# Kernel optimization log

Hardware: AMD Instinct MI355X
Metric: run time of the kernel (lower is better)

The kernel has to match this reference:

```python
import jax, jax.numpy as jnp
import numpy as np

B, N0, C, E, OUT = 64, 2048, 128, 2097152, 16


def setup_inputs() -> dict:
    key = jax.random.key(0)
    ks = jax.random.split(key, 16)
    s = 1.0 / np.sqrt(C)
    inp = {
        "x": jax.random.normal(ks[0], (B * N0, C), jnp.float32),
        "src_l": jax.random.randint(ks[1], (E,), 0, N0, jnp.int32),
        "dst_l": jax.random.randint(ks[2], (E,), 0, N0, jnp.int32),
        "g": jax.random.randint(ks[3], (E,), 0, B, jnp.int32),
    }
    for i in range(3):
        inp[f"W{i+1}"] = jax.random.normal(ks[4 + i], (C, C), jnp.float32) * s
        inp[f"b{i+1}"] = jnp.zeros((C,), jnp.float32)
        inp[f"p{i+1}"] = jax.random.normal(ks[7 + i], (C,), jnp.float32)
    inp["Wm"] = jax.random.normal(ks[10], (C, OUT), jnp.float32) * s
    inp["bm"] = jnp.zeros((OUT,), jnp.float32)
    return inp


def _gcn_conv(x, W, b, src, dst, ew, N):
    # PyG GCNConv: gcn_norm with self-loops (weight 1), symmetric D^-1/2 A D^-1/2
    xw = x @ W                                              # [N, C]
    deg = jnp.zeros((N,), xw.dtype).at[dst].add(ew) + 1.0   # +1 self-loop
    dis = jax.lax.rsqrt(deg)
    norm = dis[src] * ew * dis[dst]                         # [E]
    out = jnp.zeros_like(xw).at[dst].add(norm[:, None] * xw[src])
    out = out + xw / deg[:, None]                           # self-loop term: deg^-1
    return out + b


def _topk_pool(x, p, g, sl, dl, ew, k):
    # x: [B, n, C]; score = tanh(x.p/||p||); keep top-k nodes per graph
    n = x.shape[1]
    score = jnp.tanh(x @ (p / jnp.linalg.norm(p)))          # [B, n]
    vals, idx = jax.lax.top_k(score, k)                     # [B, k]
    xk = jnp.take_along_axis(x, idx[..., None], axis=1) * vals[..., None]
    mapping = jnp.full((x.shape[0], n), -1, jnp.int32).at[
        jnp.arange(x.shape[0])[:, None], idx
    ].set(jnp.arange(k, dtype=jnp.int32)[None, :])
    ns, nd = mapping[g, sl], mapping[g, dl]
    valid = (ew > 0) & (ns >= 0) & (nd >= 0)                # filter_adj as mask
    return xk, jnp.maximum(ns, 0), jnp.maximum(nd, 0), valid.astype(x.dtype)


def _forward(x, src_l, dst_l, g, params, Wm, bm):
    n = N0
    sl, dl = src_l, dst_l
    ew = jnp.ones(sl.shape, x.dtype)
    h = x
    for (W, b, p) in params:
        N = B * n
        src = g * n + sl
        dst = g * n + dl
        h = jax.nn.relu(_gcn_conv(h.reshape(N, -1), W, b, src, dst, ew, N))
        k = n // 2
        h, sl, dl, ew = _topk_pool(h.reshape(B, n, -1), p, g, sl, dl, ew, k)
        n = k
    pooled = h.sum(axis=1)                                  # global_add_pool -> [B, C]
    return pooled @ Wm + bm                                 # MLP([C, OUT], norm=None)


def reference(x, src_l, dst_l, g, W1, b1, p1, W2, b2, p2, W3, b3, p3, Wm, bm):
    return _forward(x, src_l, dst_l, g,
                    [(W1, b1, p1), (W2, b2, p2), (W3, b3, p3)], Wm, bm)
```

## Files before the change

### kernel.cpp

```cpp
#include <hip/hip_runtime.h>
#include <math.h>

#define BQ   64
#define NN0  2048
#define CF   128
#define ET   2097152
#define OUTF 16

static __device__ __forceinline__ unsigned f2o(float f) {
    unsigned u = __float_as_uint(f);
    return (u & 0x80000000u) ? ~u : (u | 0x80000000u);
}

__global__ void k_normp(const float* p1, const float* p2, const float* p3, float* pn) {
    const float* ps[3] = {p1, p2, p3};
    const float* p = ps[blockIdx.x];
    int t = threadIdx.x;
    float v = p[t];
    float s = v * v;
    for (int o = 32; o > 0; o >>= 1) s += __shfl_down(s, o);
    __shared__ float ws2[2];
    if ((t & 63) == 0) ws2[t >> 6] = s;
    __syncthreads();
    float tot = ws2[0] + ws2[1];
    pn[blockIdx.x * CF + t] = v / sqrtf(tot);
}

__global__ __launch_bounds__(256, 2) void k_gemm(const float* __restrict__ X,
                                                 const float* __restrict__ W,
                                                 float* __restrict__ Y, int N) {
    __shared__ float xT[32][260];
    __shared__ float Wc[32][128];
    int t = threadIdx.x;
    int cg = t & 15, rg = t >> 4;
    int c0 = cg * 8, r0 = rg * 16;
    int rowBase = blockIdx.x * 256;

    float acc[16][8];
#pragma unroll
    for (int i = 0; i < 16; i++)
#pragma unroll
        for (int j = 0; j < 8; j++) acc[i][j] = 0.f;

    for (int kc = 0; kc < 4; kc++) {
        __syncthreads();
#pragma unroll
        for (int j = 0; j < 8; j++) {
            int id = t + 256 * j;
            int r = id >> 3;
            int k4 = id & 7;
            float4 v = *(const float4*)&X[(rowBase + r) * CF + kc * 32 + k4 * 4];
            int kk = k4 * 4;
            xT[kk + 0][r] = v.x; xT[kk + 1][r] = v.y;
            xT[kk + 2][r] = v.z; xT[kk + 3][r] = v.w;
        }
#pragma unroll
        for (int j = 0; j < 4; j++) {
            int id = t + 256 * j;
            int kk = id >> 5;
            int cc = (id & 31) * 4;
            *(float4*)&Wc[kk][cc] = *(const float4*)&W[(kc * 32 + kk) * CF + cc];
        }
        __syncthreads();
#pragma unroll 4
        for (int kk = 0; kk < 32; kk++) {
            float xr[16];
#pragma unroll
            for (int i = 0; i < 16; i += 4)
                *(float4*)&xr[i] = *(float4*)&xT[kk][r0 + i];
            float wv[8];
            *(float4*)&wv[0] = *(float4*)&Wc[kk][c0];
            *(float4*)&wv[4] = *(float4*)&Wc[kk][c0 + 4];
#pragma unroll
            for (int i = 0; i < 16; i++)
#pragma unroll
                for (int j = 0; j < 8; j++)
                    acc[i][j] = fmaf(xr[i], wv[j], acc[i][j]);
        }
    }
#pragma unroll
    for (int i = 0; i < 16; i++) {
        int r = rowBase + r0 + i;
        *(float4*)&Y[r * CF + c0]     = make_float4(acc[i][0], acc[i][1], acc[i][2], acc[i][3]);
        *(float4*)&Y[r * CF + c0 + 4] = make_float4(acc[i][4], acc[i][5], acc[i][6], acc[i][7]);
    }
}

__global__ void k_hist1(const int* __restrict__ g, const int* __restrict__ dl, int* cnt) {
    int e = blockIdx.x * 256 + threadIdx.x;
    if (e < ET) atomicAdd(&cnt[g[e] * NN0 + dl[e]], 1);
}
__global__ void k_hist2(const int2* __restrict__ edges, const int* pE, int* cnt) {
    int e = blockIdx.x * 256 + threadIdx.x;
    if (e < *pE) atomicAdd(&cnt[edges[e].y], 1);
}

__global__ void k_ps1(const int* __restrict__ cnt, int* part) {
    int b = blockIdx.x, t = threadIdx.x;
    int base = b * 1024;
    int s = 0;
    for (int j = t; j < 1024; j += 256) s += cnt[base + j];
    for (int o = 32; o > 0; o >>= 1) s += __shfl_down(s, o);
    __shared__ int sm[4];
    if ((t & 63) == 0) sm[t >> 6] = s;
    __syncthreads();
    if (t == 0) part[b] = sm[0] + sm[1] + sm[2] + sm[3];
}
__global__ void k_ps3f(const int* __restrict__ cnt, const int* __restrict__ part,
                       int* rowS, int* curs, float* dis, int N, int nb) {
    __shared__ int pp[128];
    __shared__ int sm[256];
    int b = blockIdx.x, t = threadIdx.x;
    if (t < 128) pp[t] = (t < nb) ? part[t] : 0;
    __syncthreads();
    for (int o = 1; o < 128; o <<= 1) {
        int u = (t < 128 && t >= o) ? pp[t - o] : 0;
        __syncthreads();
        if (t < 128) pp[t] += u;
        __syncthreads();
    }
    int myBase = (b == 0) ? 0 : pp[b - 1];
    __syncthreads();

    int base = b * 1024;
    int loc[4], cv[4];
    int s = 0;
#pragma unroll
    for (int j = 0; j < 4; j++) { loc[j] = s; cv[j] = cnt[base + t * 4 + j]; s += cv[j]; }
    sm[t] = s;
    __syncthreads();
    for (int o = 1; o < 256; o <<= 1) {
        int u = (t >= o) ? sm[t - o] : 0;
        __syncthreads();
        sm[t] += u;
        __syncthreads();
    }
    int incl = sm[t];
    int thrBase = myBase + incl - s;
#pragma unroll
    for (int j = 0; j < 4; j++) {
        int idx = base + t * 4 + j;
        rowS[idx] = thrBase + loc[j];
        curs[idx] = thrBase + loc[j];
        if (dis != nullptr) dis[idx] = rsqrtf((float)(cv[j] + 1));
    }
    if (b == gridDim.x - 1 && t == 255) rowS[N] = myBase + incl;
}
__global__ void k_wscan(const int* __restrict__ wcnt, int* __restrict__ wbase) {
    __shared__ int sm[1024];
    int t = threadIdx.x;
    int base = t * 32;
    int v[32];
    int s = 0;
#pragma unroll
    for (int j = 0; j < 32; j++) { v[j] = s; s += wcnt[base + j]; }
    sm[t] = s;
    __syncthreads();
    for (int o = 1; o < 1024; o <<= 1) {
        int u = (t >= o) ? sm[t - o] : 0;
        __syncthreads();
        sm[t] += u;
        __syncthreads();
    }
    int ex = sm[t] - s;
#pragma unroll
    for (int j = 0; j < 32; j++) wbase[base + j] = ex + v[j];
    if (t == 1023) wbase[32768] = sm[1023];
}

__global__ void k_fill1(const int* __restrict__ g, const int* __restrict__ sl,
                        const int* __restrict__ dl, int* curs, int* csrS) {
    int r = blockIdx.x & 7;
    int base = (blockIdx.x >> 3) * 2048;
#pragma unroll
    for (int i = 0; i < 8; i++) {
        int e = base + i * 256 + threadIdx.x;
        int gg = g[e];
        int d = gg * NN0 + dl[e];
        if ((d >> 14) == r) {
            int pos = atomicAdd(&curs[d], 1);
            csrS[pos] = gg * NN0 + sl[e];
        }
    }
}
__global__ void k_fill2(const int2* __restrict__ edges, const int* pE,
                        int* curs, int* csrS, int shift) {
    int r = blockIdx.x & 7;
    int base = (blockIdx.x >> 3) * 2048;
    int E = *pE;
#pragma unroll
    for (int i = 0; i < 8; i++) {
        int e = base + i * 256 + threadIdx.x;
        if (e < E) {
            int2 ed = edges[e];
            if ((ed.y >> shift) == r) {
                int pos = atomicAdd(&curs[ed.y], 1);
                csrS[pos] = ed.x;
            }
        }
    }
}

__global__ void k_agg(const float4* __restrict__ xw, const int* __restrict__ rowS,
                      const int* __restrict__ csrS, const float* __restrict__ dis,
                      const float* __restrict__ bias, const float* __restrict__ pn,
                      float4* __restrict__ h, float* __restrict__ scores, int N) {
    int nb = gridDim.x;
    int bid = blockIdx.x;
    int sb = (bid & 7) * (nb >> 3) + (bid >> 3);
    int d = sb * 4 + (threadIdx.x >> 6);
    int lane = threadIdx.x & 63;
    int hl = lane >> 5;
    int l = lane & 31;
    int rs = rowS[d], re = rowS[d + 1];
    float4 a = make_float4(0.f, 0.f, 0.f, 0.f);
    for (int j0 = rs; j0 < re; j0 += 64) {
        int myj = j0 + lane;
        int sV = (myj < re) ? csrS[myj] : 0;
        float dV = (myj < re) ? dis[sV] : 0.f;
        int c64 = re - j0; if (c64 > 64) c64 = 64;
        int j = 0;
        for (; j + 8 <= c64; j += 8) {
            int i0 = j + hl, i1 = j + 2 + hl, i2 = j + 4 + hl, i3 = j + 6 + hl;
            int s0 = __shfl(sV, i0), s1 = __shfl(sV, i1);
            int s2 = __shfl(sV, i2), s3 = __shfl(sV, i3);
            float d0 = __shfl(dV, i0), d1 = __shfl(dV, i1);
            float d2 = __shfl(dV, i2), d3 = __shfl(dV, i3);
            float4 v0 = xw[s0 * 32 + l];
            float4 v1 = xw[s1 * 32 + l];
            float4 v2 = xw[s2 * 32 + l];
            float4 v3 = xw[s3 * 32 + l];
            a.x = fmaf(d0, v0.x, a.x); a.y = fmaf(d0, v0.y, a.y);
            a.z = fmaf(d0, v0.z, a.z); a.w = fmaf(d0, v0.w, a.w);
            a.x = fmaf(d1, v1.x, a.x); a.y = fmaf(d1, v1.y, a.y);
            a.z = fmaf(d1, v1.z, a.z); a.w = fmaf(d1, v1.w, a.w);
            a.x = fmaf(d2, v2.x, a.x); a.y = fmaf(d2, v2.y, a.y);
            a.z = fmaf(d2, v2.z, a.z); a.w = fmaf(d2, v2.w, a.w);
            a.x = fmaf(d3, v3.x, a.x); a.y = fmaf(d3, v3.y, a.y);
            a.z = fmaf(d3, v3.z, a.z); a.w = fmaf(d3, v3.w, a.w);
        }
        for (; j < c64; j += 2) {
            int i = j + hl;
            int ic = (i < c64) ? i : (c64 - 1);
            int s = __shfl(sV, ic);
            float dd = __shfl(dV, ic);
            if (i >= c64) dd = 0.f;
            float4 v = xw[s * 32 + l];
            a.x = fmaf(dd, v.x, a.x); a.y = fmaf(dd, v.y, a.y);
            a.z = fmaf(dd, v.z, a.z); a.w = fmaf(dd, v.w, a.w);
        }
    }
    a.x += __shfl_xor(a.x, 32);
    a.y += __shfl_xor(a.y, 32);
    a.z += __shfl_xor(a.z, 32);
    a.w += __shfl_xor(a.w, 32);
    float disd = dis[d];
    float invd = disd * disd;
    float4 xd = xw[d * 32 + l];
    float4 bv = ((const float4*)bias)[l];
    float4 r;
    r.x = disd * a.x + xd.x * invd + bv.x;
    r.y = disd * a.y + xd.y * invd + bv.y;
    r.z = disd * a.z + xd.z * invd + bv.z;
    r.w = disd * a.w + xd.w * invd + bv.w;
    r.x = r.x > 0.f ? r.x : 0.f;
    r.y = r.y > 0.f ? r.y : 0.f;
    r.z = r.z > 0.f ? r.z : 0.f;
    r.w = r.w > 0.f ? r.w : 0.f;
    if (hl == 0) h[d * 32 + l] = r;
    float4 pv = ((const float4*)pn)[l];
    float v = r.x * pv.x + r.y * pv.y + r.z * pv.z + r.w * pv.w;
    for (int o = 32; o > 0; o >>= 1) v += __shfl_down(v, o);
    if (lane == 0) scores[d] = tanhf(0.5f * v);
}

__global__ void k_topk(const float* __restrict__ scores, int* __restrict__ map, int n, int k) {
    __shared__ unsigned keys[2048];
    __shared__ int sm[256];
    __shared__ int red[4];
    int b = blockIdx.x, t = threadIdx.x;
    const float* sc = scores + b * n;
    int m = n >> 8;

    for (int i = t; i < n; i += 256) keys[i] = f2o(sc[i]);
    __syncthreads();

    unsigned prefix = 0u;
    for (int bit = 31; bit >= 0; bit--) {
        unsigned trial = prefix | (1u << bit);
        int c = 0;
        for (int i = t; i < n; i += 256) c += (keys[i] >= trial) ? 1 : 0;
        for (int o = 32; o > 0; o >>= 1) c += __shfl_down(c, o);
        if ((t & 63) == 0) red[t >> 6] = c;
        __syncthreads();
        int tot = red[0] + red[1] + red[2] + red[3];
        __syncthreads();
        if (tot >= k) prefix = trial;
    }
    unsigned T = prefix;

    int c = 0;
    for (int i = t; i < n; i += 256) c += (keys[i] > T) ? 1 : 0;
    for (int o = 32; o > 0; o >>= 1) c += __shfl_down(c, o);
    if ((t & 63) == 0) red[t >> 6] = c;
    __syncthreads();
    int mEq = k - (red[0] + red[1] + red[2] + red[3]);
    __syncthreads();

    int base = t * m;
    int eqc = 0;
    for (int j = 0; j < m; j++) eqc += (keys[base + j] == T) ? 1 : 0;
    sm[t] = eqc;
    __syncthreads();
    for (int o = 1; o < 256; o <<= 1) {
        int u = (t >= o) ? sm[t - o] : 0;
        __syncthreads();
        sm[t] += u;
        __syncthreads();
    }
    int er = sm[t] - eqc;
    __syncthreads();

    unsigned kb = 0; int kc = 0;
    for (int j = 0; j < m; j++) {
        unsigned ky = keys[base + j];
        bool kp = (ky > T) || (ky == T && er < mEq);
        if (ky == T) er++;
        if (kp) { kb |= (1u << j); kc++; }
    }
    sm[t] = kc;
    __syncthreads();
    for (int o = 1; o < 256; o <<= 1) {
        int u = (t >= o) ? sm[t - o] : 0;
        __syncthreads();
        sm[t] += u;
        __syncthreads();
    }
    int nidx = sm[t] - kc;
    for (int j = 0; j < m; j++) {
        map[b * n + base + j] = ((kb >> j) & 1u) ? nidx++ : -1;
    }
}

__global__ void k_compact(const float* __restrict__ h, const float* __restrict__ scores,
                          const int* __restrict__ map, float* __restrict__ xn,
                          int N, int n, int k) {
    int wid = (blockIdx.x * 256 + threadIdx.x) >> 6;
    int lane = threadIdx.x & 63;
    int mi = map[wid];
    if (mi < 0) return;
    float s = scores[wid];
    int gg = wid / n;
    int dst = (gg * k + mi) * CF;
    xn[dst + lane]      = h[wid * CF + lane] * s;
    xn[dst + 64 + lane] = h[wid * CF + 64 + lane] * s;
}

__global__ void k_remapA1(const int* __restrict__ g, const int* __restrict__ sl,
                          const int* __restrict__ dl, const int* __restrict__ map,
                          int* __restrict__ wcnt) {
    int e = blockIdx.x * 256 + threadIdx.x;
    int gg = g[e];
    bool valid = (map[gg * NN0 + sl[e]] >= 0) && (map[gg * NN0 + dl[e]] >= 0);
    unsigned long long mask = __ballot(valid);
    if ((threadIdx.x & 63) == 0) wcnt[e >> 6] = __popcll(mask);
}
__global__ void k_remapB1(const int* __restrict__ g, const int* __restrict__ sl,
                          const int* __restrict__ dl, const int* __restrict__ map,
                          const int* __restrict__ wbase, int2* __restrict__ eout,
                          int* __restrict__ pTot, int k) {
    int e = blockIdx.x * 256 + threadIdx.x;
    int lane = threadIdx.x & 63;
    int gg = g[e];
    int ns = map[gg * NN0 + sl[e]];
    int nd = map[gg * NN0 + dl[e]];
    bool valid = (ns >= 0 && nd >= 0);
    unsigned long long mask = __ballot(valid);
    if (valid) {
        int off = __popcll(mask & ((1ull << lane) - 1ull));
        eout[wbase[e >> 6] + off] = make_int2(gg * k + ns, gg * k + nd);
    }
    if (e == 0) pTot[0] = wbase[ET >> 6];
}
__global__ void k_remapA2(const int2* __restrict__ ein, const int* pE,
                          const int* __restrict__ map, int* __restrict__ wcnt) {
    int e = blockIdx.x * 256 + threadIdx.x;
    bool valid = false;
    if (e < *pE) {
        int2 ed = ein[e];
        valid = (map[ed.x] >= 0) && (map[ed.y] >= 0);
    }
    unsigned long long mask = __ballot(valid);
    if ((threadIdx.x & 63) == 0) wcnt[e >> 6] = __popcll(mask);
}
__global__ void k_remapB2(const int2* __restrict__ ein, const int* pE,
                          const int* __restrict__ map, const int* __restrict__ wbase,
                          int2* __restrict__ eout, int* __restrict__ pTot,
                          int n, int k) {
    int e = blockIdx.x * 256 + threadIdx.x;
    int lane = threadIdx.x & 63;
    bool valid = false;
    int gg = 0, ns = 0, nd = 0;
    if (e < *pE) {
        int2 ed = ein[e];
        ns = map[ed.x]; nd = map[ed.y];
        gg = ed.x / n;
        valid = (ns >= 0 && nd >= 0);
    }
    unsigned long long mask = __ballot(valid);
    if (valid) {
        int off = __popcll(mask & ((1ull << lane) - 1ull));
        eout[wbase[e >> 6] + off] = make_int2(gg * k + ns, gg * k + nd);
    }
    if (e == 0) pTot[0] = wbase[ET >> 6];
}

__global__ void k_pool3(const float* __restrict__ h, const float* __restrict__ scores,
                        const int* __restrict__ map, float* __restrict__ pooled) {
    int b = blockIdx.x, cthr = threadIdx.x;
    float acc = 0.f;
    for (int i = 0; i < 512; i++) {
        int gi = b * 512 + i;
        int mi = map[gi];
        if (mi >= 0) acc += h[gi * CF + cthr] * scores[gi];
    }
    pooled[b * CF + cthr] = acc;
}

__global__ void k_mlp(const float* __restrict__ pooled, const float* __restrict__ Wm,
                      const float* __restrict__ bm, float* __restrict__ out) {
    int b = blockIdx.x, t = threadIdx.x;
    if (t < OUTF) {
        float acc = bm[t];
        for (int c2 = 0; c2 < CF; c2++) acc += pooled[b * CF + c2] * Wm[c2 * OUTF + t];
        out[b * OUTF + t] = acc;
    }
}

extern "C" void kernel_launch(void* const* d_in, const int* in_sizes, int n_in,
                              void* d_out, int out_size, void* d_ws, size_t ws_size,
                              hipStream_t stream) {
    const float* x  = (const float*)d_in[0];
    const int* sl   = (const int*)d_in[1];
    const int* dl   = (const int*)d_in[2];
    const int* g    = (const int*)d_in[3];
    const float* W1 = (const float*)d_in[4];
    const float* b1 = (const float*)d_in[5];
    const float* p1 = (const float*)d_in[6];
    const float* W2 = (const float*)d_in[7];
    const float* b2 = (const float*)d_in[8];
    const float* p2 = (const float*)d_in[9];
    const float* W3 = (const float*)d_in[10];
    const float* b3 = (const float*)d_in[11];
    const float* p3 = (const float*)d_in[12];
    const float* Wm = (const float*)d_in[13];
    const float* bm = (const float*)d_in[14];

    char* ws = (char*)d_ws;
    float* A    = (float*)(ws + 0);
    float* Bb   = (float*)(ws + 67108864ull);
    int*   csrS = (int*)  (ws + 134217728ull);
    int*   cnt  = (int*)  (ws + 142606336ull);
    int*   rowS = (int*)  (ws + 143130624ull);
    int*   curs = (int*)  (ws + 143655168ull);
    float* scor = (float*)(ws + 144179456ull);
    int*   map  = (int*)  (ws + 144703744ull);
    float* pn   = (float*)(ws + 145228032ull);
    float* pool = (float*)(ws + 145230080ull);
    int*   ecnt = (int*)  (ws + 145262848ull);
    int*   part = (int*)  (ws + 145263104ull);
    float* dis  = (float*)(ws + 145264640ull);

    int2*  EA  = (int2*)(ws + 33554432ull);
    int2*  EB  = (int2*)(ws + 67108864ull);
    float* x2  = A;
    float* xw2 = Bb;
    float* h2  = A;
    float* x3  = (float*)(ws + 100663296ull);
    float* xw3 = A;
    float* h3  = Bb;
    int*   wcnt  = (int*)(ws + 50331648ull);
    int*   wbase = (int*)(ws + 50462720ull);

    k_normp<<<3, 128, 0, stream>>>(p1, p2, p3, pn);

    k_gemm<<<512, 256, 0, stream>>>(x, W1, A, 131072);
    hipMemsetAsync(cnt, 0, 524288, stream);
    k_hist1<<<8192, 256, 0, stream>>>(g, dl, cnt);
    k_ps1<<<128, 256, 0, stream>>>(cnt, part);
    k_ps3f<<<128, 256, 0, stream>>>(cnt, part, rowS, curs, dis, 131072, 128);
    k_fill1<<<8192, 256, 0, stream>>>(g, sl, dl, curs, csrS);
    k_agg<<<32768, 256, 0, stream>>>((const float4*)A, rowS, csrS, dis, b1, pn, (float4*)Bb, scor, 131072);
    k_topk<<<64, 256, 0, stream>>>(scor, map, 2048, 1024);
    k_compact<<<32768, 256, 0, stream>>>(Bb, scor, map, x2, 131072, 2048, 1024);
    k_remapA1<<<8192, 256, 0, stream>>>(g, sl, dl, map, wcnt);
    k_wscan<<<1, 1024, 0, stream>>>(wcnt, wbase);
    k_remapB1<<<8192, 256, 0, stream>>>(g, sl, dl, map, wbase, EA, &ecnt[0], 1024);

    k_gemm<<<256, 256, 0, stream>>>(x2, W2, xw2, 65536);
    hipMemsetAsync(cnt, 0, 262144, stream);
    k_hist2<<<8192, 256, 0, stream>>>(EA, &ecnt[0], cnt);
    k_ps1<<<64, 256, 0, stream>>>(cnt, part);
    k_ps3f<<<64, 256, 0, stream>>>(cnt, part, rowS, curs, dis, 65536, 64);
    k_fill2<<<8192, 256, 0, stream>>>(EA, &ecnt[0], curs, csrS, 13);
    k_agg<<<16384, 256, 0, stream>>>((const float4*)xw2, rowS, csrS, dis, b2, pn + 128, (float4*)h2, scor, 65536);
    k_topk<<<64, 256, 0, stream>>>(scor, map, 1024, 512);
    k_compact<<<16384, 256, 0, stream>>>(h2, scor, map, x3, 65536, 1024, 512);
    k_remapA2<<<8192, 256, 0, stream>>>(EA, &ecnt[0], map, wcnt);
    k_wscan<<<1, 1024, 0, stream>>>(wcnt, wbase);
    k_remapB2<<<8192, 256, 0, stream>>>(EA, &ecnt[0], map, wbase, EB, &ecnt[1], 1024, 512);

    k_gemm<<<128, 256, 0, stream>>>(x3, W3, xw3, 32768);
    hipMemsetAsync(cnt, 0, 131072, stream);
    k_hist2<<<8192, 256, 0, stream>>>(EB, &ecnt[1], cnt);
    k_ps1<<<32, 256, 0, stream>>>(cnt, part);
    k_ps3f<<<32, 256, 0, stream>>>(cnt, part, rowS, curs, dis, 32768, 32);
    k_fill2<<<8192, 256, 0, stream>>>(EB, &ecnt[1], curs, csrS, 12);
    k_agg<<<8192, 256, 0, stream>>>((const float4*)xw3, rowS, csrS, dis, b3, pn + 256, (float4*)h3, scor, 32768);
    k_topk<<<64, 256, 0, stream>>>(scor, map, 512, 256);
    k_pool3<<<64, 128, 0, stream>>>(h3, scor, map, pool);
    k_mlp<<<64, 64, 0, stream>>>(pool, Wm, bm, (float*)d_out);
}
```

Measured before the change: 789.5 us.

## Fuse top-k compaction into GEMM via gathered row loads

```diff
diff --git a/kernel.cpp b/kernel.cpp
--- a/kernel.cpp
+++ b/kernel.cpp
@@ -53,6 +53,70 @@
             int kk = k4 * 4;
             xT[kk + 0][r] = v.x; xT[kk + 1][r] = v.y;
             xT[kk + 2][r] = v.z; xT[kk + 3][r] = v.w;
+        }
+#pragma unroll
+        for (int j = 0; j < 4; j++) {
+            int id = t + 256 * j;
+            int kk = id >> 5;
+            int cc = (id & 31) * 4;
+            *(float4*)&Wc[kk][cc] = *(const float4*)&W[(kc * 32 + kk) * CF + cc];
+        }
+        __syncthreads();
+#pragma unroll 4
+        for (int kk = 0; kk < 32; kk++) {
+            float xr[16];
+#pragma unroll
+            for (int i = 0; i < 16; i += 4)
+                *(float4*)&xr[i] = *(float4*)&xT[kk][r0 + i];
+            float wv[8];
+            *(float4*)&wv[0] = *(float4*)&Wc[kk][c0];
+            *(float4*)&wv[4] = *(float4*)&Wc[kk][c0 + 4];
+#pragma unroll
+            for (int i = 0; i < 16; i++)
+#pragma unroll
+                for (int j = 0; j < 8; j++)
+                    acc[i][j] = fmaf(xr[i], wv[j], acc[i][j]);
+        }
+    }
+#pragma unroll
+    for (int i = 0; i < 16; i++) {
+        int r = rowBase + r0 + i;
+        *(float4*)&Y[r * CF + c0]     = make_float4(acc[i][0], acc[i][1], acc[i][2], acc[i][3]);
+        *(float4*)&Y[r * CF + c0 + 4] = make_float4(acc[i][4], acc[i][5], acc[i][6], acc[i][7]);
+    }
+}
+
+__global__ __launch_bounds__(256, 2) void k_gemmG(const float* __restrict__ H,
+                                                  const int* __restrict__ keep,
+                                                  const float* __restrict__ scor,
+                                                  const float* __restrict__ W,
+                                                  float* __restrict__ Y) {
+    __shared__ float xT[32][260];
+    __shared__ float Wc[32][128];
+    int t = threadIdx.x;
+    int cg = t & 15, rg = t >> 4;
+    int c0 = cg * 8, r0 = rg * 16;
+    int rowBase = blockIdx.x * 256;
+
+    float acc[16][8];
+#pragma unroll
+    for (int i = 0; i < 16; i++)
+#pragma unroll
+        for (int j = 0; j < 8; j++) acc[i][j] = 0.f;
+
+    for (int kc = 0; kc < 4; kc++) {
+        __syncthreads();
+#pragma unroll
+        for (int j = 0; j < 8; j++) {
+            int id = t + 256 * j;
+            int r = id >> 3;
+            int k4 = id & 7;
+            int old = keep[rowBase + r];
+            float sc = scor[old];
+            float4 v = *(const float4*)&H[old * CF + kc * 32 + k4 * 4];
+            int kk = k4 * 4;
+            xT[kk + 0][r] = v.x * sc; xT[kk + 1][r] = v.y * sc;
+            xT[kk + 2][r] = v.z * sc; xT[kk + 3][r] = v.w * sc;
         }
 #pragma unroll
         for (int j = 0; j < 4; j++) {
@@ -274,7 +338,8 @@
     if (lane == 0) scores[d] = tanhf(0.5f * v);
 }
 
-__global__ void k_topk(const float* __restrict__ scores, int* __restrict__ map, int n, int k) {
+__global__ void k_topk(const float* __restrict__ scores, int* __restrict__ map,
+                       int* __restrict__ keep, int n, int k) {
     __shared__ unsigned keys[2048];
     __shared__ int sm[256];
     __shared__ int red[4];
@@ -338,22 +403,13 @@
     }
     int nidx = sm[t] - kc;
     for (int j = 0; j < m; j++) {
-        map[b * n + base + j] = ((kb >> j) & 1u) ? nidx++ : -1;
-    }
-}
-
-__global__ void k_compact(const float* __restrict__ h, const float* __restrict__ scores,
-                          const int* __restrict__ map, float* __restrict__ xn,
-                          int N, int n, int k) {
-    int wid = (blockIdx.x * 256 + threadIdx.x) >> 6;
-    int lane = threadIdx.x & 63;
-    int mi = map[wid];
-    if (mi < 0) return;
-    float s = scores[wid];
-    int gg = wid / n;
-    int dst = (gg * k + mi) * CF;
-    xn[dst + lane]      = h[wid * CF + lane] * s;
-    xn[dst + 64 + lane] = h[wid * CF + 64 + lane] * s;
+        if ((kb >> j) & 1u) {
+            keep[b * k + nidx] = b * n + base + j;
+            map[b * n + base + j] = nidx++;
+        } else {
+            map[b * n + base + j] = -1;
+        }
+    }
 }
 
 __global__ void k_remapA1(const int* __restrict__ g, const int* __restrict__ sl,
@@ -472,15 +528,14 @@
     float* dis  = (float*)(ws + 145264640ull);
 
     int2*  EA  = (int2*)(ws + 33554432ull);
-    int2*  EB  = (int2*)(ws + 67108864ull);
-    float* x2  = A;
-    float* xw2 = Bb;
-    float* h2  = A;
-    float* x3  = (float*)(ws + 100663296ull);
+    int2*  EB  = (int2*)(ws + 100663296ull);
+    float* xw2 = A;
+    float* h2  = Bb;
     float* xw3 = A;
     float* h3  = Bb;
     int*   wcnt  = (int*)(ws + 50331648ull);
     int*   wbase = (int*)(ws + 50462720ull);
+    int*   keep  = (int*)(ws + 50724864ull);
 
     k_normp<<<3, 128, 0, stream>>>(p1, p2, p3, pn);
 
@@ -491,33 +546,31 @@
     k_ps3f<<<128, 256, 0, stream>>>(cnt, part, rowS, curs, dis, 131072, 128);
     k_fill1<<<8192, 256, 0, stream>>>(g, sl, dl, curs, csrS);
     k_agg<<<32768, 256, 0, stream>>>((const float4*)A, rowS, csrS, dis, b1, pn, (float4*)Bb, scor, 131072);
-    k_topk<<<64, 256, 0, stream>>>(scor, map, 2048, 1024);
-    k_compact<<<32768, 256, 0, stream>>>(Bb, scor, map, x2, 131072, 2048, 1024);
+    k_topk<<<64, 256, 0, stream>>>(scor, map, keep, 2048, 1024);
     k_remapA1<<<8192, 256, 0, stream>>>(g, sl, dl, map, wcnt);
     k_wscan<<<1, 1024, 0, stream>>>(wcnt, wbase);
     k_remapB1<<<8192, 256, 0, stream>>>(g, sl, dl, map, wbase, EA, &ecnt[0], 1024);
 
-    k_gemm<<<256, 256, 0, stream>>>(x2, W2, xw2, 65536);
+    k_gemmG<<<256, 256, 0, stream>>>(Bb, keep, scor, W2, xw2);
     hipMemsetAsync(cnt, 0, 262144, stream);
     k_hist2<<<8192, 256, 0, stream>>>(EA, &ecnt[0], cnt);
     k_ps1<<<64, 256, 0, stream>>>(cnt, part);
     k_ps3f<<<64, 256, 0, stream>>>(cnt, part, rowS, curs, dis, 65536, 64);
     k_fill2<<<8192, 256, 0, stream>>>(EA, &ecnt[0], curs, csrS, 13);
     k_agg<<<16384, 256, 0, stream>>>((const float4*)xw2, rowS, csrS, dis, b2, pn + 128, (float4*)h2, scor, 65536);
-    k_topk<<<64, 256, 0, stream>>>(scor, map, 1024, 512);
-    k_compact<<<16384, 256, 0, stream>>>(h2, scor, map, x3, 65536, 1024, 512);
+    k_topk<<<64, 256, 0, stream>>>(scor, map, keep, 1024, 512);
     k_remapA2<<<8192, 256, 0, stream>>>(EA, &ecnt[0], map, wcnt);
     k_wscan<<<1, 1024, 0, stream>>>(wcnt, wbase);
     k_remapB2<<<8192, 256, 0, stream>>>(EA, &ecnt[0], map, wbase, EB, &ecnt[1], 1024, 512);
 
-    k_gemm<<<128, 256, 0, stream>>>(x3, W3, xw3, 32768);
+    k_gemmG<<<128, 256, 0, stream>>>(h2, keep, scor, W3, xw3);
     hipMemsetAsync(cnt, 0, 131072, stream);
     k_hist2<<<8192, 256, 0, stream>>>(EB, &ecnt[1], cnt);
     k_ps1<<<32, 256, 0, stream>>>(cnt, part);
     k_ps3f<<<32, 256, 0, stream>>>(cnt, part, rowS, curs, dis, 32768, 32);
     k_fill2<<<8192, 256, 0, stream>>>(EB, &ecnt[1], curs, csrS, 12);
     k_agg<<<8192, 256, 0, stream>>>((const float4*)xw3, rowS, csrS, dis, b3, pn + 256, (float4*)h3, scor, 32768);
-    k_topk<<<64, 256, 0, stream>>>(scor, map, 512, 256);
+    k_topk<<<64, 256, 0, stream>>>(scor, map, keep, 512, 256);
     k_pool3<<<64, 128, 0, stream>>>(h3, scor, map, pool);
     k_mlp<<<64, 64, 0, stream>>>(pool, Wm, bm, (float*)d_out);
 }
```

Result: faster. 748.5 us (-5.2%).
